# Optimization experiments

Hardware: AMD Instinct MI355X
Metric: run time of the kernel (lower is better)

Reference implementation:

```python
import jax, jax.numpy as jnp
import numpy as np

SCALE_FACTOR = 1.0
VIS_MAX = 1024


def setup_inputs() -> dict:
    key = jax.random.key(0)
    kq, kk, kv = jax.random.split(key, 3)
    B, C, H, W = 4, 256, 64, 64
    Q = jax.random.normal(kq, (B, C, H, W), dtype=jnp.float32)
    K = jax.random.normal(kk, (B, C, H, W), dtype=jnp.float32)
    V = jax.random.normal(kv, (B, C, H, W), dtype=jnp.float32)
    return {"Q": Q, "K": K, "V": V}


def reference(Q, K, V):
    # Q,K: [B,C,H,W] -> flatten spatial dims to HW
    B, C, H, W = Q.shape
    HW = H * W
    Q_flat = Q.reshape(B, C, HW).transpose(0, 2, 1)  # [B, HW, C]
    K_flat = K.reshape(B, C, HW)                      # [B, C, HW]
    # Full scaled score matrix [B, HW, HW]; argmax over keys reproduces the
    # chunked running-max/argmax (strict '>' update keeps first max, matching
    # jnp.argmax tie-breaking).
    S = jnp.einsum('bqc,bck->bqk', Q_flat, K_flat) * SCALE_FACTOR
    H_idx = jnp.argmax(S, axis=2).astype(jnp.int64)   # [B, HW]
    vis = min(VIS_MAX, HW)
    S_vis = S[:, :vis, :vis]                          # [B, vis, vis]
    return S_vis, H_idx
```

## Files before the change

kernel.cpp:

```cpp
#include <hip/hip_runtime.h>
#include <stdint.h>

#define B_   4
#define C_   256
#define HW_  4096
#define VIS_ 1024
#define KE2  512

using half8   = __attribute__((ext_vector_type(8))) _Float16;
using floatx4 = __attribute__((ext_vector_type(4))) float;

__device__ __forceinline__ unsigned mapf(float v) {
    unsigned u = __float_as_uint(v);
    return (u & 0x80000000u) ? ~u : (u | 0x80000000u);
}

__global__ void init_ws_kernel(unsigned long long* ws, int n) {
    int i = blockIdx.x * blockDim.x + threadIdx.x;
    if (i < n) ws[i] = 0ull;
}

__global__ void finalize_kernel(const unsigned long long* __restrict__ ws,
                                float* __restrict__ out1, int n) {
    int i = blockIdx.x * blockDim.x + threadIdx.x;
    if (i < n) {
        unsigned kinv = (unsigned)(ws[i] & 0xFFFFFFFFull);
        out1[i] = (float)(HW_ - 1 - (int)kinv);
    }
}


__global__ __launch_bounds__(256) void split_transpose_kernel(
    const float* __restrict__ Q, const float* __restrict__ K,
    _Float16* __restrict__ Aexp, _Float16* __restrict__ Bexp,
    unsigned long long* __restrict__ keys)
{
    __shared__ float tile[64][65];
    const int t = threadIdx.x;
    if (blockIdx.y == 0 && blockIdx.z == 0)
        keys[blockIdx.x * 256 + t] = 0ull;

    const int hw0 = blockIdx.x * 64;
    const int c0  = blockIdx.y * 64;
    const int z = blockIdx.z, b = z >> 1, which = z & 1;
    const float* src = (which ? K : Q) + (size_t)b * C_ * HW_;
    _Float16* dst = (which ? Bexp : Aexp) + (size_t)b * HW_ * KE2;

    #pragma unroll
    for (int i = 0; i < 4; ++i) {
        int c  = (t >> 4) + i * 16;
        int hw = (t & 15) * 4;
        float4 v = *(const float4*)(src + (size_t)(c0 + c) * HW_ + hw0 + hw);
        tile[c][hw] = v.x; tile[c][hw+1] = v.y; tile[c][hw+2] = v.z; tile[c][hw+3] = v.w;
    }
    __syncthreads();

    #pragma unroll
    for (int i = 0; i < 2; ++i) {
        int id  = t + i * 256;
        int row = id >> 3;
        int c8  = (id & 7) * 8;
        half8 h8, l8;
        #pragma unroll
        for (int j = 0; j < 8; ++j) {
            float v = tile[c8 + j][row];
            _Float16 h = (_Float16)v;
            h8[j] = h;
            l8[j] = (_Float16)(v - (float)h);
        }
        _Float16* base = dst + (size_t)(hw0 + row) * KE2 + c0 + c8;
        *(half8*)(base + 0 * C_) = h8;
        *(half8*)(base + 1 * C_) = l8;
    }
}

__device__ __forceinline__ void gl2lds16(const _Float16* g, _Float16* l) {
    __builtin_amdgcn_global_load_lds(
        (const __attribute__((address_space(1))) void*)g,
        (__attribute__((address_space(3))) void*)l, 16, 0, 0);
}


#define BARRIER __builtin_amdgcn_s_barrier()
#define LGKM0   asm volatile("s_waitcnt lgkmcnt(0)" ::: "memory")
#define VMC(n)  asm volatile("s_waitcnt vmcnt(" #n ")" ::: "memory")
#define SCHEDB  __builtin_amdgcn_sched_barrier(0)

__device__ __forceinline__ void stage_half(const _Float16* __restrict__ g,
                                           _Float16* lb, int t, int kbase)
{
    #pragma unroll
    for (int j = 0; j < 2; ++j) {
        const int c   = t + j * 512;
        const int row = c >> 2;
        const int ch  = (c & 3) ^ ((row >> 1) & 3);
        gl2lds16(g + (size_t)row * KE2 + kbase + ch * 8, lb + c * 8);
    }
}

__device__ __forceinline__ void stage_chunk(const _Float16* __restrict__ Agl,
                                            const _Float16* __restrict__ Bgl,
                                            _Float16* lds, int p, int c, int t)
{
    stage_half(Agl, lds + (p * 4 + 0) * 8192, t, c * 32);
    stage_half(Agl, lds + (p * 4 + 1) * 8192, t, 256 + c * 32);
    stage_half(Bgl, lds + (p * 4 + 2) * 8192, t, c * 32);
    stage_half(Bgl, lds + (p * 4 + 3) * 8192, t, 256 + c * 32);
}

template<int MQ>
__device__ __forceinline__ void ds_load_a(const _Float16* base, int wave_m, int s,
                                          int quad, half8 (&a)[4]) {
    #pragma unroll
    for (int mi = 0; mi < 4; ++mi) {
        int row = wave_m * 128 + MQ * 64 + mi * 16 + s;
        int ch  = quad ^ ((row >> 1) & 3);
        a[mi] = *(const half8*)(base + row * 32 + ch * 8);
    }
}

__device__ __forceinline__ void ds_load_b(const _Float16* base, int wave_n, int s,
                                          int quad, half8 (&bfr)[4]) {
    #pragma unroll
    for (int ni = 0; ni < 4; ++ni) {
        int col = wave_n * 64 + ni * 16 + s;
        int ch  = quad ^ ((col >> 1) & 3);
        bfr[ni] = *(const half8*)(base + col * 32 + ch * 8);
    }
}

template<int MQ>
__device__ __forceinline__ void do_mfma(const half8 (&a)[4], const half8 (&bfr)[4],
                                        floatx4 (&acc)[8][4]) {
    __builtin_amdgcn_s_setprio(1);
    #pragma unroll
    for (int mi = 0; mi < 4; ++mi)
        #pragma unroll
        for (int ni = 0; ni < 4; ++ni)
            acc[MQ * 4 + mi][ni] = __builtin_amdgcn_mfma_f32_16x16x32_f16(
                a[mi], bfr[ni], acc[MQ * 4 + mi][ni], 0, 0, 0);
    __builtin_amdgcn_s_setprio(0);
}

__device__ __forceinline__ void chunk_compute(const _Float16* lds, int p,
    int wave_m, int wave_n, int s, int quad, floatx4 (&acc)[8][4])
{
    const _Float16* Ah = lds + (p * 4 + 0) * 8192;
    const _Float16* Al = lds + (p * 4 + 1) * 8192;
    const _Float16* Bh = lds + (p * 4 + 2) * 8192;
    const _Float16* Bl = lds + (p * 4 + 3) * 8192;
    half8 a0[4], a1[4], bh[4], bl[4];
    ds_load_a<0>(Ah, wave_m, s, quad, a0);
    ds_load_a<1>(Ah, wave_m, s, quad, a1);
    ds_load_b(Bh, wave_n, s, quad, bh);
    do_mfma<0>(a0, bh, acc);
    do_mfma<1>(a1, bh, acc);
    ds_load_b(Bl, wave_n, s, quad, bl);
    do_mfma<0>(a0, bl, acc);
    do_mfma<1>(a1, bl, acc);
    ds_load_a<0>(Al, wave_m, s, quad, a0);
    ds_load_a<1>(Al, wave_m, s, quad, a1);
    do_mfma<0>(a0, bh, acc);
    do_mfma<1>(a1, bh, acc);
}

__global__ __launch_bounds__(512, 2) void gemm_mfma_kernel(
    const _Float16* __restrict__ Aexp, const _Float16* __restrict__ Bexp,
    float* __restrict__ out0, unsigned long long* __restrict__ keys)
{
    __shared__ __align__(16) _Float16 lds[65536];

    const int t      = threadIdx.x;
    const int lane   = t & 63;
    const int wave   = t >> 6;
    const int quad   = lane >> 4;
    const int s      = lane & 15;
    const int wave_m = wave >> 2;
    const int wave_n = wave & 3;

    const int n    = blockIdx.x;
    const int wgid = (n & 7) * 128 + (n >> 3);
    const int kt   = wgid & 15;
    const int qt   = (wgid >> 4) & 15;
    const int b    = wgid >> 8;

    const _Float16* Agl = Aexp + (size_t)b * HW_ * KE2 + (size_t)(qt * 256) * KE2;
    const _Float16* Bgl = Bexp + (size_t)b * HW_ * KE2 + (size_t)(kt * 256) * KE2;

    stage_chunk(Agl, Bgl, lds, 0, 0, t);
    stage_chunk(Agl, Bgl, lds, 1, 1, t);
    VMC(8);
    BARRIER; SCHEDB;

    floatx4 acc[8][4] = {};

    #pragma unroll 1
    for (int c = 0; c < 6; ++c) {
        chunk_compute(lds, c & 1, wave_m, wave_n, s, quad, acc);
        LGKM0;
        BARRIER;
        stage_chunk(Agl, Bgl, lds, c & 1, c + 2, t);
        VMC(8);
        BARRIER; SCHEDB;
    }
    chunk_compute(lds, 0, wave_m, wave_n, s, quad, acc);
    LGKM0;
    BARRIER;
    VMC(0);
    BARRIER; SCHEDB;
    chunk_compute(lds, 1, wave_m, wave_n, s, quad, acc);

    if (qt < 4 && kt < 4) {
        #pragma unroll
        for (int mi8 = 0; mi8 < 8; ++mi8)
            #pragma unroll
            for (int r = 0; r < 4; ++r) {
                int grow = qt * 256 + wave_m * 128 + mi8 * 16 + quad * 4 + r;
                float* orow = out0 + ((size_t)b * VIS_ + grow) * VIS_ + kt * 256 + wave_n * 64;
                #pragma unroll
                for (int ni = 0; ni < 4; ++ni)
                    orow[ni * 16 + s] = acc[mi8][ni][r];
            }
    }

    __syncthreads();
    unsigned long long* red = (unsigned long long*)lds;

    #pragma unroll
    for (int mi8 = 0; mi8 < 8; ++mi8) {
        #pragma unroll
        for (int r = 0; r < 4; ++r) {
            float best = acc[mi8][0][r];
            int bcol = wave_n * 64 + s;
            #pragma unroll
            for (int ni = 1; ni < 4; ++ni) {
                float v = acc[mi8][ni][r];
                if (v > best) { best = v; bcol = wave_n * 64 + ni * 16 + s; }
            }
            int gcol = kt * 256 + bcol;
            unsigned long long key = ((unsigned long long)mapf(best) << 32)
                                   | (unsigned)(HW_ - 1 - gcol);
            #pragma unroll
            for (int m = 1; m < 16; m <<= 1) {
                unsigned long long o = __shfl_xor(key, m, 64);
                if (o > key) key = o;
            }
            if (s == 0)
                red[(wave_m * 128 + mi8 * 16 + quad * 4 + r) * 4 + wave_n] = key;
        }
    }
    __syncthreads();
    if (t < 256) {
        const unsigned long long* rr = red + t * 4;
        unsigned long long k0 = rr[0], k1 = rr[1], k2 = rr[2], k3 = rr[3];
        unsigned long long m01 = k0 > k1 ? k0 : k1;
        unsigned long long m23 = k2 > k3 ? k2 : k3;
        atomicMax(&keys[(size_t)b * HW_ + qt * 256 + t], m01 > m23 ? m01 : m23);
    }
}

#define BT   64
#define BK   32
#define LDP  68

__global__ __launch_bounds__(256) void gemm_argmax_kernel(
    const float* __restrict__ Q, const float* __restrict__ K,
    float* __restrict__ out0, unsigned long long* __restrict__ ws)
{
    __shared__ float As[BK][LDP];
    __shared__ float Bs[BK][LDP];
    __shared__ unsigned long long red[BT][17];

    const int t  = threadIdx.x;
    const int tx = t & 15;
    const int ty = t >> 4;
    const int k0 = blockIdx.x * BT;
    const int q0 = blockIdx.y * BT;
    const int b  = blockIdx.z;

    const float* Qb = Q + (size_t)b * C_ * HW_;
    const float* Kb = K + (size_t)b * C_ * HW_;

    float acc[4][4] = {{0.f},{0.f},{0.f},{0.f}};

    for (int c0 = 0; c0 < C_; c0 += BK) {
        #pragma unroll
        for (int i = 0; i < 2; ++i) {
            int idx = i * 256 + t;
            int row = idx >> 4;
            int col = (idx & 15) * 4;
            const float4 a  = *(const float4*)(Qb + (size_t)(c0 + row) * HW_ + q0 + col);
            const float4 bv = *(const float4*)(Kb + (size_t)(c0 + row) * HW_ + k0 + col);
            *(float4*)(&As[row][col]) = a;
            *(float4*)(&Bs[row][col]) = bv;
        }
        __syncthreads();
        #pragma unroll
        for (int cc = 0; cc < BK; ++cc) {
            const float4 av = *(const float4*)(&As[cc][ty * 4]);
            const float4 bv = *(const float4*)(&Bs[cc][tx * 4]);
            const float a_[4] = {av.x, av.y, av.z, av.w};
            const float b_[4] = {bv.x, bv.y, bv.z, bv.w};
            #pragma unroll
            for (int i = 0; i < 4; ++i)
                #pragma unroll
                for (int j = 0; j < 4; ++j)
                    acc[i][j] = fmaf(a_[i], b_[j], acc[i][j]);
        }
        __syncthreads();
    }

    if (q0 < VIS_ && k0 < VIS_) {
        #pragma unroll
        for (int i = 0; i < 4; ++i) {
            float4 v = make_float4(acc[i][0], acc[i][1], acc[i][2], acc[i][3]);
            size_t off = (size_t)b * VIS_ * VIS_ + (size_t)(q0 + ty * 4 + i) * VIS_ + (k0 + tx * 4);
            *(float4*)(out0 + off) = v;
        }
    }

    #pragma unroll
    for (int i = 0; i < 4; ++i) {
        float best = acc[i][0];
        int   bj   = 0;
        #pragma unroll
        for (int j = 1; j < 4; ++j)
            if (acc[i][j] > best) { best = acc[i][j]; bj = j; }
        int kidx = k0 + tx * 4 + bj;
        unsigned long long key = ((unsigned long long)mapf(best) << 32)
                               | (unsigned)(HW_ - 1 - kidx);
        red[ty * 4 + i][tx] = key;
    }
    __syncthreads();
    if (t < BT) {
        unsigned long long best = red[t][0];
        #pragma unroll
        for (int j = 1; j < 16; ++j) {
            unsigned long long v = red[t][j];
            if (v > best) best = v;
        }
        atomicMax(&ws[(size_t)b * HW_ + q0 + t], best);
    }
}

extern "C" void kernel_launch(void* const* d_in, const int* in_sizes, int n_in,
                              void* d_out, int out_size, void* d_ws, size_t ws_size,
                              hipStream_t stream) {
    const float* Q = (const float*)d_in[0];
    const float* K = (const float*)d_in[1];
    float* out0 = (float*)d_out;
    float* out1 = out0 + (size_t)B_ * VIS_ * VIS_;

    unsigned long long* keys = (unsigned long long*)d_ws;
    const size_t keys_bytes = (size_t)B_ * HW_ * 8;
    const size_t exp_elems  = (size_t)B_ * HW_ * KE2;
    const size_t need = keys_bytes + 2 * exp_elems * sizeof(_Float16);

    const int n = B_ * HW_;

    if (ws_size >= need) {
        _Float16* Aexp = (_Float16*)((char*)d_ws + keys_bytes);
        _Float16* Bexp = Aexp + exp_elems;
        split_transpose_kernel<<<dim3(HW_ / 64, C_ / 64, 2 * B_), 256, 0, stream>>>(Q, K, Aexp, Bexp, keys);
        gemm_mfma_kernel<<<dim3((HW_ / 256) * (HW_ / 256) * B_), 512, 0, stream>>>(Aexp, Bexp, out0, keys);
    } else {
        init_ws_kernel<<<(n + 255) / 256, 256, 0, stream>>>(keys, n);
        gemm_argmax_kernel<<<dim3(HW_ / BT, HW_ / BT, B_), 256, 0, stream>>>(Q, K, out0, keys);
    }

    finalize_kernel<<<(n + 255) / 256, 256, 0, stream>>>(keys, out1, n);
}
```

Baseline: 208.1 us.

## Fuse fp16 split conversion into GEMM staging, dropping the pre-transpose kernel

```diff
diff --git a/kernel.cpp b/kernel.cpp
--- a/kernel.cpp
+++ b/kernel.cpp
@@ -5,7 +5,6 @@
 #define C_   256
 #define HW_  4096
 #define VIS_ 1024
-#define KE2  512
 
 using half8   = __attribute__((ext_vector_type(8))) _Float16;
 using floatx4 = __attribute__((ext_vector_type(4))) float;
@@ -30,82 +29,56 @@
 }
 
 
-__global__ __launch_bounds__(256) void split_transpose_kernel(
-    const float* __restrict__ Q, const float* __restrict__ K,
-    _Float16* __restrict__ Aexp, _Float16* __restrict__ Bexp,
-    unsigned long long* __restrict__ keys)
-{
-    __shared__ float tile[64][65];
-    const int t = threadIdx.x;
-    if (blockIdx.y == 0 && blockIdx.z == 0)
-        keys[blockIdx.x * 256 + t] = 0ull;
-
-    const int hw0 = blockIdx.x * 64;
-    const int c0  = blockIdx.y * 64;
-    const int z = blockIdx.z, b = z >> 1, which = z & 1;
-    const float* src = (which ? K : Q) + (size_t)b * C_ * HW_;
-    _Float16* dst = (which ? Bexp : Aexp) + (size_t)b * HW_ * KE2;
-
-    #pragma unroll
-    for (int i = 0; i < 4; ++i) {
-        int c  = (t >> 4) + i * 16;
-        int hw = (t & 15) * 4;
-        float4 v = *(const float4*)(src + (size_t)(c0 + c) * HW_ + hw0 + hw);
-        tile[c][hw] = v.x; tile[c][hw+1] = v.y; tile[c][hw+2] = v.z; tile[c][hw+3] = v.w;
-    }
-    __syncthreads();
-
-    #pragma unroll
-    for (int i = 0; i < 2; ++i) {
-        int id  = t + i * 256;
-        int row = id >> 3;
-        int c8  = (id & 7) * 8;
-        half8 h8, l8;
-        #pragma unroll
-        for (int j = 0; j < 8; ++j) {
-            float v = tile[c8 + j][row];
-            _Float16 h = (_Float16)v;
-            h8[j] = h;
-            l8[j] = (_Float16)(v - (float)h);
-        }
-        _Float16* base = dst + (size_t)(hw0 + row) * KE2 + c0 + c8;
-        *(half8*)(base + 0 * C_) = h8;
-        *(half8*)(base + 1 * C_) = l8;
-    }
-}
-
-__device__ __forceinline__ void gl2lds16(const _Float16* g, _Float16* l) {
-    __builtin_amdgcn_global_load_lds(
-        (const __attribute__((address_space(1))) void*)g,
-        (__attribute__((address_space(3))) void*)l, 16, 0, 0);
-}
-
-
 #define BARRIER __builtin_amdgcn_s_barrier()
 #define LGKM0   asm volatile("s_waitcnt lgkmcnt(0)" ::: "memory")
-#define VMC(n)  asm volatile("s_waitcnt vmcnt(" #n ")" ::: "memory")
 #define SCHEDB  __builtin_amdgcn_sched_barrier(0)
 
-__device__ __forceinline__ void stage_half(const _Float16* __restrict__ g,
-                                           _Float16* lb, int t, int kbase)
-{
-    #pragma unroll
-    for (int j = 0; j < 2; ++j) {
-        const int c   = t + j * 512;
-        const int row = c >> 2;
-        const int ch  = (c & 3) ^ ((row >> 1) & 3);
-        gl2lds16(g + (size_t)row * KE2 + kbase + ch * 8, lb + c * 8);
-    }
-}
-
-__device__ __forceinline__ void stage_chunk(const _Float16* __restrict__ Agl,
-                                            const _Float16* __restrict__ Bgl,
-                                            _Float16* lds, int p, int c, int t)
-{
-    stage_half(Agl, lds + (p * 4 + 0) * 8192, t, c * 32);
-    stage_half(Agl, lds + (p * 4 + 1) * 8192, t, 256 + c * 32);
-    stage_half(Bgl, lds + (p * 4 + 2) * 8192, t, c * 32);
-    stage_half(Bgl, lds + (p * 4 + 3) * 8192, t, 256 + c * 32);
+__device__ __forceinline__ void stage_load(const float* __restrict__ Qp,
+                                           const float* __restrict__ Kp,
+                                           int kb, int t,
+                                           float (&ra)[2][8], float (&rb)[2][8])
+{
+    const int hw = t & 255, o0 = t >> 8;
+    #pragma unroll
+    for (int k = 0; k < 2; ++k) {
+        const int c0 = kb + (o0 + 2 * k) * 8;
+        const float* qa = Qp + (size_t)c0 * HW_ + hw;
+        const float* ka = Kp + (size_t)c0 * HW_ + hw;
+        #pragma unroll
+        for (int j = 0; j < 8; ++j) {
+            ra[k][j] = qa[(size_t)j * HW_];
+            rb[k][j] = ka[(size_t)j * HW_];
+        }
+    }
+}
+
+__device__ __forceinline__ void cvt_write(_Float16* lds, int p, int t,
+                                          const float (&ra)[2][8],
+                                          const float (&rb)[2][8])
+{
+    _Float16* Ah = lds + (p * 4 + 0) * 8192;
+    _Float16* Al = lds + (p * 4 + 1) * 8192;
+    _Float16* Bh = lds + (p * 4 + 2) * 8192;
+    _Float16* Bl = lds + (p * 4 + 3) * 8192;
+    const int hw = t & 255, o0 = t >> 8, swz = (hw >> 1) & 3;
+    #pragma unroll
+    for (int k = 0; k < 2; ++k) {
+        const int ch = (o0 + 2 * k) ^ swz;
+        half8 ha, la, hb, lb;
+        #pragma unroll
+        for (int j = 0; j < 8; ++j) {
+            float v = ra[k][j];
+            _Float16 h = (_Float16)v;
+            ha[j] = h; la[j] = (_Float16)(v - (float)h);
+            float w = rb[k][j];
+            _Float16 g = (_Float16)w;
+            hb[j] = g; lb[j] = (_Float16)(w - (float)g);
+        }
+        *(half8*)(Ah + hw * 32 + ch * 8) = ha;
+        *(half8*)(Al + hw * 32 + ch * 8) = la;
+        *(half8*)(Bh + hw * 32 + ch * 8) = hb;
+        *(half8*)(Bl + hw * 32 + ch * 8) = lb;
+    }
 }
 
 template<int MQ>
@@ -149,23 +122,23 @@
     const _Float16* Al = lds + (p * 4 + 1) * 8192;
     const _Float16* Bh = lds + (p * 4 + 2) * 8192;
     const _Float16* Bl = lds + (p * 4 + 3) * 8192;
-    half8 a0[4], a1[4], bh[4], bl[4];
-    ds_load_a<0>(Ah, wave_m, s, quad, a0);
-    ds_load_a<1>(Ah, wave_m, s, quad, a1);
+    half8 bh[4], bl[4], a[4];
     ds_load_b(Bh, wave_n, s, quad, bh);
-    do_mfma<0>(a0, bh, acc);
-    do_mfma<1>(a1, bh, acc);
     ds_load_b(Bl, wave_n, s, quad, bl);
-    do_mfma<0>(a0, bl, acc);
-    do_mfma<1>(a1, bl, acc);
-    ds_load_a<0>(Al, wave_m, s, quad, a0);
-    ds_load_a<1>(Al, wave_m, s, quad, a1);
-    do_mfma<0>(a0, bh, acc);
-    do_mfma<1>(a1, bh, acc);
+    ds_load_a<0>(Ah, wave_m, s, quad, a);
+    do_mfma<0>(a, bh, acc);
+    do_mfma<0>(a, bl, acc);
+    ds_load_a<1>(Ah, wave_m, s, quad, a);
+    do_mfma<1>(a, bh, acc);
+    do_mfma<1>(a, bl, acc);
+    ds_load_a<0>(Al, wave_m, s, quad, a);
+    do_mfma<0>(a, bh, acc);
+    ds_load_a<1>(Al, wave_m, s, quad, a);
+    do_mfma<1>(a, bh, acc);
 }
 
 __global__ __launch_bounds__(512, 2) void gemm_mfma_kernel(
-    const _Float16* __restrict__ Aexp, const _Float16* __restrict__ Bexp,
+    const float* __restrict__ Q, const float* __restrict__ K,
     float* __restrict__ out0, unsigned long long* __restrict__ keys)
 {
     __shared__ __align__(16) _Float16 lds[65536];
@@ -184,30 +157,29 @@
     const int qt   = (wgid >> 4) & 15;
     const int b    = wgid >> 8;
 
-    const _Float16* Agl = Aexp + (size_t)b * HW_ * KE2 + (size_t)(qt * 256) * KE2;
-    const _Float16* Bgl = Bexp + (size_t)b * HW_ * KE2 + (size_t)(kt * 256) * KE2;
-
-    stage_chunk(Agl, Bgl, lds, 0, 0, t);
-    stage_chunk(Agl, Bgl, lds, 1, 1, t);
-    VMC(8);
-    BARRIER; SCHEDB;
+    const float* Qp = Q + (size_t)b * C_ * HW_ + qt * 256;
+    const float* Kp = K + (size_t)b * C_ * HW_ + kt * 256;
+
+    float ra[2][8], rb[2][8];
+
+    stage_load(Qp, Kp, 0, t, ra, rb);
+    cvt_write(lds, 0, t, ra, rb);
+    stage_load(Qp, Kp, 32, t, ra, rb);
+    cvt_write(lds, 1, t, ra, rb);
+    stage_load(Qp, Kp, 64, t, ra, rb);
+    LGKM0; BARRIER; SCHEDB;
 
     floatx4 acc[8][4] = {};
 
     #pragma unroll 1
     for (int c = 0; c < 6; ++c) {
         chunk_compute(lds, c & 1, wave_m, wave_n, s, quad, acc);
-        LGKM0;
-        BARRIER;
-        stage_chunk(Agl, Bgl, lds, c & 1, c + 2, t);
-        VMC(8);
-        BARRIER; SCHEDB;
+        LGKM0; BARRIER;
+        cvt_write(lds, c & 1, t, ra, rb);
+        if (c < 5) stage_load(Qp, Kp, (c + 3) * 32, t, ra, rb);
+        LGKM0; BARRIER; SCHEDB;
     }
     chunk_compute(lds, 0, wave_m, wave_n, s, quad, acc);
-    LGKM0;
-    BARRIER;
-    VMC(0);
-    BARRIER; SCHEDB;
     chunk_compute(lds, 1, wave_m, wave_n, s, quad, acc);
 
     if (qt < 4 && kt < 4) {
@@ -353,18 +325,13 @@
 
     unsigned long long* keys = (unsigned long long*)d_ws;
     const size_t keys_bytes = (size_t)B_ * HW_ * 8;
-    const size_t exp_elems  = (size_t)B_ * HW_ * KE2;
-    const size_t need = keys_bytes + 2 * exp_elems * sizeof(_Float16);
 
     const int n = B_ * HW_;
-
-    if (ws_size >= need) {
-        _Float16* Aexp = (_Float16*)((char*)d_ws + keys_bytes);
-        _Float16* Bexp = Aexp + exp_elems;
-        split_transpose_kernel<<<dim3(HW_ / 64, C_ / 64, 2 * B_), 256, 0, stream>>>(Q, K, Aexp, Bexp, keys);
-        gemm_mfma_kernel<<<dim3((HW_ / 256) * (HW_ / 256) * B_), 512, 0, stream>>>(Aexp, Bexp, out0, keys);
+    init_ws_kernel<<<(n + 255) / 256, 256, 0, stream>>>(keys, n);
+
+    if (ws_size >= keys_bytes) {
+        gemm_mfma_kernel<<<dim3((HW_ / 256) * (HW_ / 256) * B_), 512, 0, stream>>>(Q, K, out0, keys);
     } else {
-        init_ws_kernel<<<(n + 255) / 256, 256, 0, stream>>>(keys, n);
         gemm_argmax_kernel<<<dim3(HW_ / BT, HW_ / BT, B_), 256, 0, stream>>>(Q, K, out0, keys);
     }
 
```

Result: no change. 206.4 us (-0.8%).
